# Optimization experiments

Hardware: AMD Instinct MI355X
Metric: run time of the kernel (lower is better)

Reference implementation:

```python
import jax, jax.numpy as jnp
import numpy as np

E = 8        # n_experts
TOP_K = 2    # n_activated_experts
B, T, C = 4, 2048, 2048   # batch, seq, d_model
F = 5632     # expert FFN hidden (SwiGLU)


def setup_inputs() -> dict:
    key = jax.random.key(0)
    k = jax.random.split(key, 5)
    s = 0.02  # init scale keeps activations sane
    return {
        "x":  jax.random.normal(k[0], (B, T, C), jnp.float32),
        "Wg": jax.random.normal(k[1], (C, E), jnp.float32) * s,   # gate Linear (no bias)
        "W1": jax.random.normal(k[2], (E, C, F), jnp.float32) * s, # expert gate proj
        "W3": jax.random.normal(k[3], (E, C, F), jnp.float32) * s, # expert up proj
        "W2": jax.random.normal(k[4], (E, F, C), jnp.float32) * s, # expert down proj
    }


def _moe(x, Wg, W1, W3, W2, top_k=TOP_K, norm_probs=True):
    Bb, Tt, Cc = x.shape
    xf = x.reshape(-1, Cc)                                   # [N, C]
    logits = xf @ Wg                                         # [N, E]
    probs = jax.nn.softmax(logits.astype(jnp.float32), axis=-1)
    probs, indices = jax.lax.top_k(probs, top_k)             # [N, K]
    if norm_probs:
        probs = probs / probs.sum(axis=-1, keepdims=True)
    probs = probs.astype(x.dtype)
    N, Ee = xf.shape[0], W1.shape[0]
    # per-token combine weights: w[n, e] = prob if expert e selected for token n else 0
    # (top_k indices are distinct per token, so at most one add per (n, e))
    w = jnp.zeros((N, Ee), x.dtype).at[jnp.arange(N)[:, None], indices].add(probs)
    # scan over experts: weight-0 tokens contribute nothing, matching the sparse
    # masked dispatch/scatter-add of the original exactly.
    def body(y, ws):
        w1, w3, w2, we = ws                                   # we: [N]
        h = jax.nn.silu(xf @ w1) * (xf @ w3)                  # [N, F]
        return y + we[:, None] * (h @ w2), None
    y, _ = jax.lax.scan(body, jnp.zeros_like(xf), (W1, W3, W2, w.T))
    return y.reshape(Bb, Tt, Cc)


def reference(x, Wg, W1, W3, W2):
    return _moe(x, Wg, W1, W3, W2)
```

## Files before the change

### kernel.cpp

```cpp
#include <hip/hip_runtime.h>

#define N_TOK 8192
#define C_DIM 2048
#define F_DIM 5632
#define E_NUM 8
#define BK 64

#define BM 256
#define MAXT 72
#define BN1 128
#define GRID1 (MAXT * (F_DIM/BN1))
#define BN2 256
#define KSPLIT 2
#define GRID2 (MAXT * (C_DIM/BN2) * KSPLIT)
#define NT1 (C_DIM/BK)
#define NT2H (F_DIM/BK/KSPLIT)
#define KHALF (F_DIM/KSPLIT)

typedef __attribute__((ext_vector_type(8))) short bf16x8;
typedef __attribute__((ext_vector_type(4))) float f32x4;

typedef const void __attribute__((address_space(1)))* gas1;
typedef void __attribute__((address_space(3)))* las3;

__device__ __forceinline__ unsigned short f2bf(float f){
  union { float f; unsigned u; } v; v.f = f;
  unsigned r = v.u + 0x7FFFu + ((v.u >> 16) & 1u);
  return (unsigned short)(r >> 16);
}

__device__ __forceinline__ void glds16(const unsigned short* g, unsigned short* l){
  __builtin_amdgcn_global_load_lds((gas1)g, (las3)l, 16, 0, 0);
}

#define MFMA_BF16 __builtin_amdgcn_mfma_f32_16x16x32_bf16

__global__ void k_tcvt_w(const float* __restrict__ inA, const float* __restrict__ inB,
                         unsigned short* __restrict__ out, int R, int Cc){
  __shared__ float t[64][65];
  int z = blockIdx.z;
  const float* in = (z < 8 ? inA : inB) + (size_t)(z & 7) * R * Cc;
  out += (size_t)z * R * Cc;
  int c0 = blockIdx.x * 64, r0 = blockIdx.y * 64;
  int tx = threadIdx.x, ty = threadIdx.y;
  #pragma unroll
  for (int i = 0; i < 16; ++i){
    int r = ty + i*4;
    t[r][tx] = in[(size_t)(r0 + r) * Cc + c0 + tx];
  }
  __syncthreads();
  #pragma unroll
  for (int i = 0; i < 16; ++i){
    int cr = ty + i*4;
    out[(size_t)(c0 + cr) * R + r0 + tx] = f2bf(t[tx][cr]);
  }
}

__global__ void k_router(const float* __restrict__ x, const float* __restrict__ Wg,
                         int* __restrict__ cnt, int* __restrict__ list, float* __restrict__ p_slot,
                         unsigned short* __restrict__ xb)
{
  int wid = threadIdx.x >> 6, lane = threadIdx.x & 63;
  int n = blockIdx.x * 4 + wid;
  int e = lane >> 3, sub = lane & 7;
  const float* xr = x + (size_t)n * C_DIM;
  float acc = 0.f;
  for (int i0 = sub*4; i0 < C_DIM; i0 += 32){
    float4 v = *(const float4*)&xr[i0];
    acc += v.x * Wg[(i0  )*E_NUM + e];
    acc += v.y * Wg[(i0+1)*E_NUM + e];
    acc += v.z * Wg[(i0+2)*E_NUM + e];
    acc += v.w * Wg[(i0+3)*E_NUM + e];
  }
  acc += __shfl_xor(acc, 1);
  acc += __shfl_xor(acc, 2);
  acc += __shfl_xor(acc, 4);
  float lg[E_NUM];
  #pragma unroll
  for (int j = 0; j < E_NUM; ++j) lg[j] = __shfl(acc, j*8);
  unsigned short* xbr = xb + (size_t)n * C_DIM;
  #pragma unroll
  for (int i0 = lane*4; i0 < C_DIM; i0 += 256){
    float4 v = *(const float4*)&xr[i0];
    ushort4 u; u.x = f2bf(v.x); u.y = f2bf(v.y); u.z = f2bf(v.z); u.w = f2bf(v.w);
    *(ushort4*)&xbr[i0] = u;
  }
  if (lane == 0){
    int e1 = 0; float m1 = lg[0];
    #pragma unroll
    for (int j = 1; j < E_NUM; ++j) if (lg[j] > m1){ m1 = lg[j]; e1 = j; }
    int e2 = -1; float m2 = -1e30f;
    #pragma unroll
    for (int j = 0; j < E_NUM; ++j) if (j != e1 && lg[j] > m2){ m2 = lg[j]; e2 = j; }
    float p1 = 1.f / (1.f + __expf(m2 - m1));
    float p2 = 1.f - p1;
    int pos1 = atomicAdd(&cnt[e1], 1);
    list[e1*N_TOK + pos1] = n*2;
    p_slot[n*2] = p1;
    int pos2 = atomicAdd(&cnt[e2], 1);
    list[e2*N_TOK + pos2] = n*2 + 1;
    p_slot[n*2 + 1] = p2;
  }
}

__global__ void k_prefix(const int* __restrict__ cnt, int* __restrict__ meta){
  if (threadIdx.x == 0 && blockIdx.x == 0){
    int acc = 0, t = 0;
    for (int e = 0; e < E_NUM; ++e){
      meta[e] = acc; acc += cnt[e];
      int nt = (cnt[e] + BM - 1) / BM;
      for (int i = 0; i < nt; ++i) meta[16 + t++] = (e << 16) | i;
    }
    meta[8] = t;
  }
}

#define PHASE_ENTER() do{ __builtin_amdgcn_sched_barrier(0); __builtin_amdgcn_s_barrier(); \
                          __builtin_amdgcn_s_setprio(1); } while(0)
#define PHASE_EXIT()  do{ __builtin_amdgcn_s_setprio(0); __builtin_amdgcn_sched_barrier(0); \
                          __builtin_amdgcn_s_barrier(); } while(0)

__global__ __launch_bounds__(512, 2) void k_gemm1(
    const unsigned short* __restrict__ xb,
    const unsigned short* __restrict__ wb1,
    const unsigned short* __restrict__ wb3,
    unsigned short* __restrict__ h,
    const int* __restrict__ cnt,
    const int* __restrict__ meta,
    const int* __restrict__ list)
{
  int o = blockIdx.x;
  int w = (o & 7) * (GRID1/8) + (o >> 3);
  int t = w % MAXT;
  int n0 = (w / MAXT) * BN1;
  if (t >= meta[8]) return;
  int info = meta[16 + t];
  int e  = info >> 16;
  int m0 = (info & 0xffff) * BM;
  int count = cnt[e];
  int hbase = meta[e];

  __shared__ __align__(16) unsigned short lds[2*32768];

  int tid = threadIdx.x;
  int lane = tid & 63, wid = tid >> 6;
  int wm = wid >> 1, wn = wid & 1;
  int l15 = lane & 15;
  int xc0 = (lane >> 4) ^ (lane & 7);
  int xc1 = xc0 ^ 4;

  int srow = tid >> 3;
  int swz = ((tid & 7) ^ (srow & 7)) * 8;
  const unsigned short* aP[4];
  #pragma unroll
  for (int u = 0; u < 4; ++u){
    int ts = list[e*N_TOK + m0 + u*64 + srow];
    int tok = (ts >> 1) & (N_TOK - 1);
    aP[u] = xb + (size_t)tok * C_DIM + swz;
  }
  const unsigned short* bP[4];
  #pragma unroll
  for (int u = 0; u < 4; ++u){
    const unsigned short* base = (u < 2) ? wb1 : wb3;
    bP[u] = base + ((size_t)e*F_DIM + n0 + (u & 1)*64 + srow) * C_DIM + swz;
  }
  int ldw = wid * 512;

  #define ST_A(u, kt) glds16(aP[u] + (kt)*BK, &lds[((kt)&1)*32768 + (u)*4096 + ldw])
  #define ST_B(u, kt) glds16(bP[u] + (kt)*BK, &lds[((kt)&1)*32768 + 16384 + (u)*4096 + ldw])

  ST_A(0,0); ST_A(1,0); ST_A(2,0); ST_A(3,0);
  ST_B(0,0); ST_B(1,0); ST_B(2,0); ST_B(3,0);
  ST_A(0,1); ST_A(1,1); ST_A(2,1); ST_A(3,1);
  asm volatile("s_waitcnt vmcnt(4)" ::: "memory");
  __builtin_amdgcn_sched_barrier(0);
  __builtin_amdgcn_s_barrier();

  f32x4 zero = {0.f, 0.f, 0.f, 0.f};
  f32x4 acc1[4][4], acc3[4][4];
  #pragma unroll
  for (int m = 0; m < 4; ++m)
    #pragma unroll
    for (int q = 0; q < 4; ++q){ acc1[m][q] = zero; acc3[m][q] = zero; }

  for (int kt = 0; kt < NT1; ++kt){
    const unsigned short* bufc = &lds[(kt & 1)*32768];
    bf16x8 a[4][2], b1f[2], b3f[2];
    #pragma unroll
    for (int m = 0; m < 4; ++m){
      int row = wm*64 + m*16 + l15;
      a[m][0] = *(const bf16x8*)&bufc[row*64 + xc0*8];
      a[m][1] = *(const bf16x8*)&bufc[row*64 + xc1*8];
    }
    {
      int brow = wn*64 + l15;
      b1f[0] = *(const bf16x8*)&bufc[16384 + brow*64 + xc0*8];
      b1f[1] = *(const bf16x8*)&bufc[16384 + brow*64 + xc1*8];
      b3f[0] = *(const bf16x8*)&bufc[24576 + brow*64 + xc0*8];
      b3f[1] = *(const bf16x8*)&bufc[24576 + brow*64 + xc1*8];
    }
    ST_B(0, kt+1); ST_B(1, kt+1); ST_B(2, kt+1); ST_B(3, kt+1);
    PHASE_ENTER();
    #pragma unroll
    for (int m = 0; m < 4; ++m){
      acc1[m][0] = MFMA_BF16(a[m][0], b1f[0], acc1[m][0], 0, 0, 0);
      acc1[m][0] = MFMA_BF16(a[m][1], b1f[1], acc1[m][0], 0, 0, 0);
      acc3[m][0] = MFMA_BF16(a[m][0], b3f[0], acc3[m][0], 0, 0, 0);
      acc3[m][0] = MFMA_BF16(a[m][1], b3f[1], acc3[m][0], 0, 0, 0);
    }
    PHASE_EXIT();
    #pragma unroll
    for (int q = 1; q < 4; ++q){
      int brow = wn*64 + q*16 + l15;
      b1f[0] = *(const bf16x8*)&bufc[16384 + brow*64 + xc0*8];
      b1f[1] = *(const bf16x8*)&bufc[16384 + brow*64 + xc1*8];
      b3f[0] = *(const bf16x8*)&bufc[24576 + brow*64 + xc0*8];
      b3f[1] = *(const bf16x8*)&bufc[24576 + brow*64 + xc1*8];
      if (q == 1){ ST_A(0, kt+2); ST_A(1, kt+2); }
      if (q == 2){ ST_A(2, kt+2); ST_A(3, kt+2); }
      PHASE_ENTER();
      #pragma unroll
      for (int m = 0; m < 4; ++m){
        acc1[m][q] = MFMA_BF16(a[m][0], b1f[0], acc1[m][q], 0, 0, 0);
        acc1[m][q] = MFMA_BF16(a[m][1], b1f[1], acc1[m][q], 0, 0, 0);
        acc3[m][q] = MFMA_BF16(a[m][0], b3f[0], acc3[m][q], 0, 0, 0);
        acc3[m][q] = MFMA_BF16(a[m][1], b3f[1], acc3[m][q], 0, 0, 0);
      }
      __builtin_amdgcn_s_setprio(0);
      if (q == 3) asm volatile("s_waitcnt vmcnt(4)" ::: "memory");
      __builtin_amdgcn_sched_barrier(0);
      __builtin_amdgcn_s_barrier();
    }
  }
  asm volatile("s_waitcnt vmcnt(0)" ::: "memory");

  #pragma unroll
  for (int m = 0; m < 4; ++m){
    #pragma unroll
    for (int r = 0; r < 4; ++r){
      int rloc = m0 + wm*64 + m*16 + ((lane >> 4) * 4) + r;
      if (rloc < count){
        unsigned short* hrow = h + (size_t)(hbase + rloc) * F_DIM + n0 + wn*64 + l15;
        #pragma unroll
        for (int q = 0; q < 4; ++q){
          float v1 = acc1[m][q][r];
          float v3 = acc3[m][q][r];
          float hv = (v1 / (1.f + __expf(-v1))) * v3;
          hrow[q*16] = f2bf(hv);
        }
      }
    }
  }
  #undef ST_A
  #undef ST_B
}

__global__ __launch_bounds__(512, 2) void k_gemm2(
    const unsigned short* __restrict__ h,
    const unsigned short* __restrict__ wb2,
    float* __restrict__ y,
    const int* __restrict__ cnt,
    const int* __restrict__ meta,
    const int* __restrict__ list,
    const float* __restrict__ p_slot)
{
  int o = blockIdx.x;
  int w = (o & 7) * (GRID2/8) + (o >> 3);
  int ks = w / (GRID2/KSPLIT);
  int r2 = w % (GRID2/KSPLIT);
  int t = r2 % MAXT;
  int n0 = (r2 / MAXT) * BN2;
  if (t >= meta[8]) return;
  int info = meta[16 + t];
  int e  = info >> 16;
  int m0 = (info & 0xffff) * BM;
  int count = cnt[e];
  int hbase = meta[e];

  __shared__ __align__(16) unsigned short lds[2*32768];

  int tid = threadIdx.x;
  int lane = tid & 63, wid = tid >> 6;
  int wm = wid >> 1, wn = wid & 1;
  int l15 = lane & 15;
  int xc0 = (lane >> 4) ^ (lane & 7);
  int xc1 = xc0 ^ 4;

  int srow = tid >> 3;
  int swz = ((tid & 7) ^ (srow & 7)) * 8;
  size_t kb0 = (size_t)ks * KHALF;
  const unsigned short* aP[4];
  #pragma unroll
  for (int u = 0; u < 4; ++u)
    aP[u] = h + (size_t)(hbase + m0 + u*64 + srow) * F_DIM + kb0 + swz;
  const unsigned short* bP[4];
  #pragma unroll
  for (int u = 0; u < 4; ++u)
    bP[u] = wb2 + ((size_t)e*C_DIM + n0 + u*64 + srow) * F_DIM + kb0 + swz;
  int ldw = wid * 512;

  #define ST_A2(u, kt) glds16(aP[u] + (kt)*BK, &lds[((kt)&1)*32768 + (u)*4096 + ldw])
  #define ST_B2(u, kt) glds16(bP[u] + (kt)*BK, &lds[((kt)&1)*32768 + 16384 + (u)*4096 + ldw])

  ST_A2(0,0); ST_A2(1,0); ST_A2(2,0); ST_A2(3,0);
  ST_B2(0,0); ST_B2(1,0); ST_B2(2,0); ST_B2(3,0);
  asm volatile("s_waitcnt vmcnt(4)" ::: "memory");
  ST_A2(0,1); ST_A2(1,1); ST_A2(2,1); ST_A2(3,1);
  ST_B2(0,1); ST_B2(2,1);
  asm volatile("s_waitcnt vmcnt(6)" ::: "memory");
  __builtin_amdgcn_sched_barrier(0);
  __builtin_amdgcn_s_barrier();

  f32x4 zero = {0.f, 0.f, 0.f, 0.f};
  f32x4 acc[4][8];
  #pragma unroll
  for (int m = 0; m < 4; ++m)
    #pragma unroll
    for (int nf = 0; nf < 8; ++nf) acc[m][nf] = zero;

  for (int kt = 0; kt < NT2H; ++kt){
    const unsigned short* bufc = &lds[(kt & 1)*32768];
    bf16x8 a[4][2], bf[2][2];
    #pragma unroll
    for (int m = 0; m < 4; ++m){
      int row = wm*64 + m*16 + l15;
      a[m][0] = *(const bf16x8*)&bufc[row*64 + xc0*8];
      a[m][1] = *(const bf16x8*)&bufc[row*64 + xc1*8];
    }
    #pragma unroll
    for (int j = 0; j < 2; ++j){
      int brow = wn*128 + j*16 + l15;
      bf[j][0] = *(const bf16x8*)&bufc[16384 + brow*64 + xc0*8];
      bf[j][1] = *(const bf16x8*)&bufc[16384 + brow*64 + xc1*8];
    }
    ST_B2(1, kt+1); ST_B2(3, kt+1);
    PHASE_ENTER();
    #pragma unroll
    for (int m = 0; m < 4; ++m)
      #pragma unroll
      for (int j = 0; j < 2; ++j){
        acc[m][j] = MFMA_BF16(a[m][0], bf[j][0], acc[m][j], 0, 0, 0);
        acc[m][j] = MFMA_BF16(a[m][1], bf[j][1], acc[m][j], 0, 0, 0);
      }
    PHASE_EXIT();
    #pragma unroll
    for (int q = 1; q < 4; ++q){
      #pragma unroll
      for (int j = 0; j < 2; ++j){
        int brow = wn*128 + (q*2 + j)*16 + l15;
        bf[j][0] = *(const bf16x8*)&bufc[16384 + brow*64 + xc0*8];
        bf[j][1] = *(const bf16x8*)&bufc[16384 + brow*64 + xc1*8];
      }
      if (q == 1){ ST_A2(0, kt+2); ST_A2(1, kt+2); }
      if (q == 2){ ST_A2(2, kt+2); ST_A2(3, kt+2); }
      if (q == 3){ ST_B2(0, kt+2); ST_B2(2, kt+2); }
      PHASE_ENTER();
      #pragma unroll
      for (int m = 0; m < 4; ++m)
        #pragma unroll
        for (int j = 0; j < 2; ++j){
          acc[m][q*2+j] = MFMA_BF16(a[m][0], bf[j][0], acc[m][q*2+j], 0, 0, 0);
          acc[m][q*2+j] = MFMA_BF16(a[m][1], bf[j][1], acc[m][q*2+j], 0, 0, 0);
        }
      __builtin_amdgcn_s_setprio(0);
      if (q == 3) asm volatile("s_waitcnt vmcnt(6)" ::: "memory");
      __builtin_amdgcn_sched_barrier(0);
      __builtin_amdgcn_s_barrier();
    }
  }
  asm volatile("s_waitcnt vmcnt(0)" ::: "memory");

  #pragma unroll
  for (int m = 0; m < 4; ++m){
    #pragma unroll
    for (int r = 0; r < 4; ++r){
      int rloc = m0 + wm*64 + m*16 + ((lane >> 4) * 4) + r;
      if (rloc < count){
        int ts = list[e*N_TOK + rloc];
        float p = p_slot[ts];
        int tok = ts >> 1;
        float* yr = y + (size_t)tok * C_DIM + n0 + wn*128 + l15;
        #pragma unroll
        for (int nf = 0; nf < 8; ++nf)
          atomicAdd(&yr[nf*16], p * acc[m][nf][r]);
      }
    }
  }
  #undef ST_A2
  #undef ST_B2
}

extern "C" void kernel_launch(void* const* d_in, const int* in_sizes, int n_in,
                              void* d_out, int out_size, void* d_ws, size_t ws_size,
                              hipStream_t stream)
{
  const float* x  = (const float*)d_in[0];
  const float* Wg = (const float*)d_in[1];
  const float* W1 = (const float*)d_in[2];
  const float* W3 = (const float*)d_in[3];
  const float* W2 = (const float*)d_in[4];
  float* y = (float*)d_out;
  (void)in_sizes; (void)n_in; (void)out_size; (void)ws_size;

  char* ws = (char*)d_ws;
  size_t o = 0;
  auto alloc = [&](size_t bytes)->char* {
    char* p = ws + o;
    o = (o + bytes + 255) & ~(size_t)255;
    return p;
  };
  int*    cnt    = (int*)  alloc(E_NUM * 4);
  int*    meta   = (int*)  alloc(160 * 4);
  float*  p_slot = (float*)alloc((size_t)2*N_TOK * 4);
  int*    list   = (int*)  alloc((size_t)E_NUM*N_TOK * 4);
  unsigned short* xb  = (unsigned short*)alloc((size_t)N_TOK*C_DIM * 2);
  unsigned short* wb1 = (unsigned short*)alloc((size_t)E_NUM*C_DIM*F_DIM * 2);
  unsigned short* wb3 = (unsigned short*)alloc((size_t)E_NUM*C_DIM*F_DIM * 2);
  unsigned short* wb2 = (unsigned short*)alloc((size_t)E_NUM*C_DIM*F_DIM * 2);
  unsigned short* h   = (unsigned short*)alloc((size_t)(2*N_TOK + 1024)*F_DIM * 2);
  (void)wb3;

  hipMemsetAsync(cnt, 0, E_NUM * 4, stream);
  hipMemsetAsync(y, 0, (size_t)N_TOK * C_DIM * 4, stream);
  k_router<<<N_TOK/4, 256, 0, stream>>>(x, Wg, cnt, list, p_slot, xb);
  k_prefix<<<1, 64, 0, stream>>>(cnt, meta);
  k_tcvt_w<<<dim3(F_DIM/64, C_DIM/64, 2*E_NUM), dim3(64,4), 0, stream>>>(W1, W3, wb1, C_DIM, F_DIM);
  k_tcvt_w<<<dim3(C_DIM/64, F_DIM/64, E_NUM), dim3(64,4), 0, stream>>>(W2, W2, wb2, F_DIM, C_DIM);
  k_gemm1<<<GRID1, 512, 0, stream>>>(xb, wb1, wb3, h, cnt, meta, list);
  k_gemm2<<<GRID2, 512, 0, stream>>>(h, wb2, y, cnt, meta, list, p_slot);
}
```

Baseline: 1.834 ms.

## Fuse preprocessing kernels, overlap W2 conversion with GEMM1, prefetch A fragments

The router, the y zeroing and the W1/W3 transpose-convert now run as one launch, replacing a memset and three kernels. The W2 transpose-convert is appended as extra blocks of the GEMM1 grid so it can overlap with the expert GEMM work. Both GEMM main loops now load the next tile's A fragments from LDS during the last sub-phase and carry them in registers across iterations, which adds register pressure and moves one B prefetch in GEMM2. Packing the conversion blocks after the GEMM blocks depends on the block scheduler running them alongside the GEMM blocks.

```diff
diff --git a/kernel.cpp b/kernel.cpp
--- a/kernel.cpp
+++ b/kernel.cpp
@@ -17,6 +17,13 @@
 #define NT2H (F_DIM/BK/KSPLIT)
 #define KHALF (F_DIM/KSPLIT)
 
+#define PRE_R 2048
+#define PRE_Y 4096
+#define PRE_T 45056
+#define GRID_PRE (PRE_R + PRE_Y + PRE_T)
+#define G1_TCVT 22528
+#define GRID1F (GRID1 + G1_TCVT)
+
 typedef __attribute__((ext_vector_type(8))) short bf16x8;
 typedef __attribute__((ext_vector_type(4))) float f32x4;
 
@@ -35,71 +42,87 @@
 
 #define MFMA_BF16 __builtin_amdgcn_mfma_f32_16x16x32_bf16
 
-__global__ void k_tcvt_w(const float* __restrict__ inA, const float* __restrict__ inB,
-                         unsigned short* __restrict__ out, int R, int Cc){
+__global__ __launch_bounds__(256) void k_pre(
+    const float* __restrict__ x, const float* __restrict__ Wg,
+    const float* __restrict__ W1, const float* __restrict__ W3,
+    int* __restrict__ cnt, int* __restrict__ list, float* __restrict__ p_slot,
+    unsigned short* __restrict__ xb, unsigned short* __restrict__ wb13,
+    float* __restrict__ y)
+{
   __shared__ float t[64][65];
-  int z = blockIdx.z;
-  const float* in = (z < 8 ? inA : inB) + (size_t)(z & 7) * R * Cc;
-  out += (size_t)z * R * Cc;
-  int c0 = blockIdx.x * 64, r0 = blockIdx.y * 64;
-  int tx = threadIdx.x, ty = threadIdx.y;
+  int bid = blockIdx.x;
+  int tid = threadIdx.x;
+
+  if (bid < PRE_R){
+    int wid = tid >> 6, lane = tid & 63;
+    int n = bid * 4 + wid;
+    int e = lane >> 3, sub = lane & 7;
+    const float* xr = x + (size_t)n * C_DIM;
+    float acc = 0.f;
+    for (int i0 = sub*4; i0 < C_DIM; i0 += 32){
+      float4 v = *(const float4*)&xr[i0];
+      acc += v.x * Wg[(i0  )*E_NUM + e];
+      acc += v.y * Wg[(i0+1)*E_NUM + e];
+      acc += v.z * Wg[(i0+2)*E_NUM + e];
+      acc += v.w * Wg[(i0+3)*E_NUM + e];
+    }
+    acc += __shfl_xor(acc, 1);
+    acc += __shfl_xor(acc, 2);
+    acc += __shfl_xor(acc, 4);
+    float lg[E_NUM];
+    #pragma unroll
+    for (int j = 0; j < E_NUM; ++j) lg[j] = __shfl(acc, j*8);
+    unsigned short* xbr = xb + (size_t)n * C_DIM;
+    #pragma unroll
+    for (int i0 = lane*4; i0 < C_DIM; i0 += 256){
+      float4 v = *(const float4*)&xr[i0];
+      ushort4 u; u.x = f2bf(v.x); u.y = f2bf(v.y); u.z = f2bf(v.z); u.w = f2bf(v.w);
+      *(ushort4*)&xbr[i0] = u;
+    }
+    if (lane == 0){
+      int e1 = 0; float m1 = lg[0];
+      #pragma unroll
+      for (int j = 1; j < E_NUM; ++j) if (lg[j] > m1){ m1 = lg[j]; e1 = j; }
+      int e2 = -1; float m2 = -1e30f;
+      #pragma unroll
+      for (int j = 0; j < E_NUM; ++j) if (j != e1 && lg[j] > m2){ m2 = lg[j]; e2 = j; }
+      float p1 = 1.f / (1.f + __expf(m2 - m1));
+      float p2 = 1.f - p1;
+      int pos1 = atomicAdd(&cnt[e1], 1);
+      list[e1*N_TOK + pos1] = n*2;
+      p_slot[n*2] = p1;
+      int pos2 = atomicAdd(&cnt[e2], 1);
+      list[e2*N_TOK + pos2] = n*2 + 1;
+      p_slot[n*2 + 1] = p2;
+    }
+    return;
+  }
+  if (bid < PRE_R + PRE_Y){
+    float4* y4 = (float4*)y;
+    size_t base = (size_t)(bid - PRE_R) * 1024 + tid;
+    float4 z4 = {0.f, 0.f, 0.f, 0.f};
+    #pragma unroll
+    for (int j = 0; j < 4; ++j) y4[base + j*256] = z4;
+    return;
+  }
+  int rel = bid - (PRE_R + PRE_Y);
+  int z = rel / 2816;
+  int r2 = rel - z*2816;
+  int fx = r2 % 88, cy = r2 / 88;
+  const float* in = ((z < 8) ? W1 : W3) + (size_t)(z & 7) * C_DIM * F_DIM;
+  unsigned short* out = wb13 + (size_t)z * C_DIM * F_DIM;
+  int c0 = fx*64, r0 = cy*64;
+  int tx = tid & 63, ty = tid >> 6;
   #pragma unroll
   for (int i = 0; i < 16; ++i){
     int r = ty + i*4;
-    t[r][tx] = in[(size_t)(r0 + r) * Cc + c0 + tx];
+    t[r][tx] = in[(size_t)(r0 + r) * F_DIM + c0 + tx];
   }
   __syncthreads();
   #pragma unroll
   for (int i = 0; i < 16; ++i){
     int cr = ty + i*4;
-    out[(size_t)(c0 + cr) * R + r0 + tx] = f2bf(t[tx][cr]);
-  }
-}
-
-__global__ void k_router(const float* __restrict__ x, const float* __restrict__ Wg,
-                         int* __restrict__ cnt, int* __restrict__ list, float* __restrict__ p_slot,
-                         unsigned short* __restrict__ xb)
-{
-  int wid = threadIdx.x >> 6, lane = threadIdx.x & 63;
-  int n = blockIdx.x * 4 + wid;
-  int e = lane >> 3, sub = lane & 7;
-  const float* xr = x + (size_t)n * C_DIM;
-  float acc = 0.f;
-  for (int i0 = sub*4; i0 < C_DIM; i0 += 32){
-    float4 v = *(const float4*)&xr[i0];
-    acc += v.x * Wg[(i0  )*E_NUM + e];
-    acc += v.y * Wg[(i0+1)*E_NUM + e];
-    acc += v.z * Wg[(i0+2)*E_NUM + e];
-    acc += v.w * Wg[(i0+3)*E_NUM + e];
-  }
-  acc += __shfl_xor(acc, 1);
-  acc += __shfl_xor(acc, 2);
-  acc += __shfl_xor(acc, 4);
-  float lg[E_NUM];
-  #pragma unroll
-  for (int j = 0; j < E_NUM; ++j) lg[j] = __shfl(acc, j*8);
-  unsigned short* xbr = xb + (size_t)n * C_DIM;
-  #pragma unroll
-  for (int i0 = lane*4; i0 < C_DIM; i0 += 256){
-    float4 v = *(const float4*)&xr[i0];
-    ushort4 u; u.x = f2bf(v.x); u.y = f2bf(v.y); u.z = f2bf(v.z); u.w = f2bf(v.w);
-    *(ushort4*)&xbr[i0] = u;
-  }
-  if (lane == 0){
-    int e1 = 0; float m1 = lg[0];
-    #pragma unroll
-    for (int j = 1; j < E_NUM; ++j) if (lg[j] > m1){ m1 = lg[j]; e1 = j; }
-    int e2 = -1; float m2 = -1e30f;
-    #pragma unroll
-    for (int j = 0; j < E_NUM; ++j) if (j != e1 && lg[j] > m2){ m2 = lg[j]; e2 = j; }
-    float p1 = 1.f / (1.f + __expf(m2 - m1));
-    float p2 = 1.f - p1;
-    int pos1 = atomicAdd(&cnt[e1], 1);
-    list[e1*N_TOK + pos1] = n*2;
-    p_slot[n*2] = p1;
-    int pos2 = atomicAdd(&cnt[e2], 1);
-    list[e2*N_TOK + pos2] = n*2 + 1;
-    p_slot[n*2 + 1] = p2;
+    out[(size_t)(c0 + cr) * C_DIM + r0 + tx] = f2bf(t[tx][cr]);
   }
 }
 
@@ -127,9 +150,38 @@
     unsigned short* __restrict__ h,
     const int* __restrict__ cnt,
     const int* __restrict__ meta,
-    const int* __restrict__ list)
+    const int* __restrict__ list,
+    const float* __restrict__ W2,
+    unsigned short* __restrict__ wb2)
 {
+  __shared__ __align__(16) unsigned short lds[2*32768];
   int o = blockIdx.x;
+  int tid = threadIdx.x;
+
+  if (o >= GRID1){
+    float (*t)[65] = (float(*)[65])lds;
+    int rel = o - GRID1;
+    int z = rel / 2816;
+    int r2 = rel - z*2816;
+    int cx = r2 % 32, fy = r2 / 32;
+    const float* in = W2 + (size_t)z * F_DIM * C_DIM;
+    unsigned short* out = wb2 + (size_t)z * C_DIM * F_DIM;
+    int c0 = cx*64, r0 = fy*64;
+    int tx = tid & 63, ty = tid >> 6;
+    #pragma unroll
+    for (int i = 0; i < 8; ++i){
+      int r = ty + i*8;
+      t[r][tx] = in[(size_t)(r0 + r) * C_DIM + c0 + tx];
+    }
+    __syncthreads();
+    #pragma unroll
+    for (int i = 0; i < 8; ++i){
+      int cr = ty + i*8;
+      out[(size_t)(c0 + cr) * F_DIM + r0 + tx] = f2bf(t[tx][cr]);
+    }
+    return;
+  }
+
   int w = (o & 7) * (GRID1/8) + (o >> 3);
   int t = w % MAXT;
   int n0 = (w / MAXT) * BN1;
@@ -140,9 +192,6 @@
   int count = cnt[e];
   int hbase = meta[e];
 
-  __shared__ __align__(16) unsigned short lds[2*32768];
-
-  int tid = threadIdx.x;
   int lane = tid & 63, wid = tid >> 6;
   int wm = wid >> 1, wn = wid & 1;
   int l15 = lane & 15;
@@ -183,15 +232,18 @@
     #pragma unroll
     for (int q = 0; q < 4; ++q){ acc1[m][q] = zero; acc3[m][q] = zero; }
 
+  bf16x8 a[4][2];
+  #pragma unroll
+  for (int m = 0; m < 4; ++m){
+    int row = wm*64 + m*16 + l15;
+    a[m][0] = *(const bf16x8*)&lds[row*64 + xc0*8];
+    a[m][1] = *(const bf16x8*)&lds[row*64 + xc1*8];
+  }
+
   for (int kt = 0; kt < NT1; ++kt){
     const unsigned short* bufc = &lds[(kt & 1)*32768];
-    bf16x8 a[4][2], b1f[2], b3f[2];
-    #pragma unroll
-    for (int m = 0; m < 4; ++m){
-      int row = wm*64 + m*16 + l15;
-      a[m][0] = *(const bf16x8*)&bufc[row*64 + xc0*8];
-      a[m][1] = *(const bf16x8*)&bufc[row*64 + xc1*8];
-    }
+    const unsigned short* bufn = &lds[((kt+1) & 1)*32768];
+    bf16x8 b1f[2], b3f[2];
     {
       int brow = wn*64 + l15;
       b1f[0] = *(const bf16x8*)&bufc[16384 + brow*64 + xc0*8];
@@ -210,14 +262,14 @@
     }
     PHASE_EXIT();
     #pragma unroll
-    for (int q = 1; q < 4; ++q){
+    for (int q = 1; q < 3; ++q){
       int brow = wn*64 + q*16 + l15;
       b1f[0] = *(const bf16x8*)&bufc[16384 + brow*64 + xc0*8];
       b1f[1] = *(const bf16x8*)&bufc[16384 + brow*64 + xc1*8];
       b3f[0] = *(const bf16x8*)&bufc[24576 + brow*64 + xc0*8];
       b3f[1] = *(const bf16x8*)&bufc[24576 + brow*64 + xc1*8];
       if (q == 1){ ST_A(0, kt+2); ST_A(1, kt+2); }
-      if (q == 2){ ST_A(2, kt+2); ST_A(3, kt+2); }
+      else       { ST_A(2, kt+2); ST_A(3, kt+2); }
       PHASE_ENTER();
       #pragma unroll
       for (int m = 0; m < 4; ++m){
@@ -226,11 +278,36 @@
         acc3[m][q] = MFMA_BF16(a[m][0], b3f[0], acc3[m][q], 0, 0, 0);
         acc3[m][q] = MFMA_BF16(a[m][1], b3f[1], acc3[m][q], 0, 0, 0);
       }
-      __builtin_amdgcn_s_setprio(0);
-      if (q == 3) asm volatile("s_waitcnt vmcnt(4)" ::: "memory");
-      __builtin_amdgcn_sched_barrier(0);
-      __builtin_amdgcn_s_barrier();
-    }
+      PHASE_EXIT();
+    }
+    {
+      int brow = wn*64 + 3*16 + l15;
+      b1f[0] = *(const bf16x8*)&bufc[16384 + brow*64 + xc0*8];
+      b1f[1] = *(const bf16x8*)&bufc[16384 + brow*64 + xc1*8];
+      b3f[0] = *(const bf16x8*)&bufc[24576 + brow*64 + xc0*8];
+      b3f[1] = *(const bf16x8*)&bufc[24576 + brow*64 + xc1*8];
+    }
+    asm volatile("s_waitcnt vmcnt(4)" ::: "memory");
+    __builtin_amdgcn_sched_barrier(0);
+    __builtin_amdgcn_s_barrier();
+    __builtin_amdgcn_s_setprio(1);
+    bf16x8 an[4][2];
+    #pragma unroll
+    for (int m = 0; m < 4; ++m){
+      int row = wm*64 + m*16 + l15;
+      an[m][0] = *(const bf16x8*)&bufn[row*64 + xc0*8];
+      an[m][1] = *(const bf16x8*)&bufn[row*64 + xc1*8];
+    }
+    #pragma unroll
+    for (int m = 0; m < 4; ++m){
+      acc1[m][3] = MFMA_BF16(a[m][0], b1f[0], acc1[m][3], 0, 0, 0);
+      acc1[m][3] = MFMA_BF16(a[m][1], b1f[1], acc1[m][3], 0, 0, 0);
+      acc3[m][3] = MFMA_BF16(a[m][0], b3f[0], acc3[m][3], 0, 0, 0);
+      acc3[m][3] = MFMA_BF16(a[m][1], b3f[1], acc3[m][3], 0, 0, 0);
+    }
+    PHASE_EXIT();
+    #pragma unroll
+    for (int m = 0; m < 4; ++m){ a[m][0] = an[m][0]; a[m][1] = an[m][1]; }
   }
   asm volatile("s_waitcnt vmcnt(0)" ::: "memory");
 
@@ -318,15 +395,18 @@
     #pragma unroll
     for (int nf = 0; nf < 8; ++nf) acc[m][nf] = zero;
 
+  bf16x8 a[4][2];
+  #pragma unroll
+  for (int m = 0; m < 4; ++m){
+    int row = wm*64 + m*16 + l15;
+    a[m][0] = *(const bf16x8*)&lds[row*64 + xc0*8];
+    a[m][1] = *(const bf16x8*)&lds[row*64 + xc1*8];
+  }
+
   for (int kt = 0; kt < NT2H; ++kt){
     const unsigned short* bufc = &lds[(kt & 1)*32768];
-    bf16x8 a[4][2], bf[2][2];
-    #pragma unroll
-    for (int m = 0; m < 4; ++m){
-      int row = wm*64 + m*16 + l15;
-      a[m][0] = *(const bf16x8*)&bufc[row*64 + xc0*8];
-      a[m][1] = *(const bf16x8*)&bufc[row*64 + xc1*8];
-    }
+    const unsigned short* bufn = &lds[((kt+1) & 1)*32768];
+    bf16x8 bf[2][2];
     #pragma unroll
     for (int j = 0; j < 2; ++j){
       int brow = wn*128 + j*16 + l15;
@@ -344,7 +424,7 @@
       }
     PHASE_EXIT();
     #pragma unroll
-    for (int q = 1; q < 4; ++q){
+    for (int q = 1; q < 3; ++q){
       #pragma unroll
       for (int j = 0; j < 2; ++j){
         int brow = wn*128 + (q*2 + j)*16 + l15;
@@ -352,8 +432,7 @@
         bf[j][1] = *(const bf16x8*)&bufc[16384 + brow*64 + xc1*8];
       }
       if (q == 1){ ST_A2(0, kt+2); ST_A2(1, kt+2); }
-      if (q == 2){ ST_A2(2, kt+2); ST_A2(3, kt+2); }
-      if (q == 3){ ST_B2(0, kt+2); ST_B2(2, kt+2); }
+      else       { ST_A2(2, kt+2); ST_A2(3, kt+2); }
       PHASE_ENTER();
       #pragma unroll
       for (int m = 0; m < 4; ++m)
@@ -362,11 +441,36 @@
           acc[m][q*2+j] = MFMA_BF16(a[m][0], bf[j][0], acc[m][q*2+j], 0, 0, 0);
           acc[m][q*2+j] = MFMA_BF16(a[m][1], bf[j][1], acc[m][q*2+j], 0, 0, 0);
         }
-      __builtin_amdgcn_s_setprio(0);
-      if (q == 3) asm volatile("s_waitcnt vmcnt(6)" ::: "memory");
-      __builtin_amdgcn_sched_barrier(0);
-      __builtin_amdgcn_s_barrier();
-    }
+      PHASE_EXIT();
+    }
+    #pragma unroll
+    for (int j = 0; j < 2; ++j){
+      int brow = wn*128 + (6 + j)*16 + l15;
+      bf[j][0] = *(const bf16x8*)&bufc[16384 + brow*64 + xc0*8];
+      bf[j][1] = *(const bf16x8*)&bufc[16384 + brow*64 + xc1*8];
+    }
+    ST_B2(0, kt+2); ST_B2(2, kt+2);
+    asm volatile("s_waitcnt vmcnt(6)" ::: "memory");
+    __builtin_amdgcn_sched_barrier(0);
+    __builtin_amdgcn_s_barrier();
+    __builtin_amdgcn_s_setprio(1);
+    bf16x8 an[4][2];
+    #pragma unroll
+    for (int m = 0; m < 4; ++m){
+      int row = wm*64 + m*16 + l15;
+      an[m][0] = *(const bf16x8*)&bufn[row*64 + xc0*8];
+      an[m][1] = *(const bf16x8*)&bufn[row*64 + xc1*8];
+    }
+    #pragma unroll
+    for (int m = 0; m < 4; ++m)
+      #pragma unroll
+      for (int j = 0; j < 2; ++j){
+        acc[m][6+j] = MFMA_BF16(a[m][0], bf[j][0], acc[m][6+j], 0, 0, 0);
+        acc[m][6+j] = MFMA_BF16(a[m][1], bf[j][1], acc[m][6+j], 0, 0, 0);
+      }
+    PHASE_EXIT();
+    #pragma unroll
+    for (int m = 0; m < 4; ++m){ a[m][0] = an[m][0]; a[m][1] = an[m][1]; }
   }
   asm volatile("s_waitcnt vmcnt(0)" ::: "memory");
 
@@ -421,11 +525,8 @@
   (void)wb3;
 
   hipMemsetAsync(cnt, 0, E_NUM * 4, stream);
-  hipMemsetAsync(y, 0, (size_t)N_TOK * C_DIM * 4, stream);
-  k_router<<<N_TOK/4, 256, 0, stream>>>(x, Wg, cnt, list, p_slot, xb);
+  k_pre<<<GRID_PRE, 256, 0, stream>>>(x, Wg, W1, W3, cnt, list, p_slot, xb, wb1, y);
   k_prefix<<<1, 64, 0, stream>>>(cnt, meta);
-  k_tcvt_w<<<dim3(F_DIM/64, C_DIM/64, 2*E_NUM), dim3(64,4), 0, stream>>>(W1, W3, wb1, C_DIM, F_DIM);
-  k_tcvt_w<<<dim3(C_DIM/64, F_DIM/64, E_NUM), dim3(64,4), 0, stream>>>(W2, W2, wb2, F_DIM, C_DIM);
-  k_gemm1<<<GRID1, 512, 0, stream>>>(xb, wb1, wb3, h, cnt, meta, list);
+  k_gemm1<<<GRID1F, 512, 0, stream>>>(xb, wb1, wb3, h, cnt, meta, list, W2, wb2);
   k_gemm2<<<GRID2, 512, 0, stream>>>(h, wb2, y, cnt, meta, list, p_slot);
 }
```

After: 1.842 ms. Within noise of the previous version (+0.5%).

## Fuse router, output zeroing and W1/W3 transpose; software-pipeline LDS fragment reads in GEMMs

Applied to the files above, without the earlier changes.

Merges the router, the y memset and the W1/W3 bf16 transpose into one launch, so these independent prep jobs can run concurrently and launch overhead drops. In both GEMM kernels, the LDS fragment reads are now double-buffered in registers: the next B slice (and the next tile's A) is read while MFMAs run on the current one. This hides LDS latency behind matrix math, at the cost of more live registers, which may pressure occupancy under the 512x2 launch bounds.

```diff
diff --git a/kernel.cpp b/kernel.cpp
--- a/kernel.cpp
+++ b/kernel.cpp
@@ -17,6 +17,11 @@
 #define NT2H (F_DIM/BK/KSPLIT)
 #define KHALF (F_DIM/KSPLIT)
 
+#define PRE_R 2048
+#define PRE_Y 4096
+#define PRE_T 45056
+#define GRID_PRE (PRE_R + PRE_Y + PRE_T)
+
 typedef __attribute__((ext_vector_type(8))) short bf16x8;
 typedef __attribute__((ext_vector_type(4))) float f32x4;
 
@@ -35,71 +40,106 @@
 
 #define MFMA_BF16 __builtin_amdgcn_mfma_f32_16x16x32_bf16
 
-__global__ void k_tcvt_w(const float* __restrict__ inA, const float* __restrict__ inB,
-                         unsigned short* __restrict__ out, int R, int Cc){
+__global__ __launch_bounds__(256) void k_pre(
+    const float* __restrict__ x, const float* __restrict__ Wg,
+    const float* __restrict__ W1, const float* __restrict__ W3,
+    int* __restrict__ cnt, int* __restrict__ list, float* __restrict__ p_slot,
+    unsigned short* __restrict__ xb, unsigned short* __restrict__ wb13,
+    float* __restrict__ y)
+{
   __shared__ float t[64][65];
-  int z = blockIdx.z;
-  const float* in = (z < 8 ? inA : inB) + (size_t)(z & 7) * R * Cc;
-  out += (size_t)z * R * Cc;
+  int bid = blockIdx.x;
+  int tid = threadIdx.x;
+
+  if (bid < PRE_R){
+    int wid = tid >> 6, lane = tid & 63;
+    int n = bid * 4 + wid;
+    int e = lane >> 3, sub = lane & 7;
+    const float* xr = x + (size_t)n * C_DIM;
+    float acc = 0.f;
+    for (int i0 = sub*4; i0 < C_DIM; i0 += 32){
+      float4 v = *(const float4*)&xr[i0];
+      acc += v.x * Wg[(i0  )*E_NUM + e];
+      acc += v.y * Wg[(i0+1)*E_NUM + e];
+      acc += v.z * Wg[(i0+2)*E_NUM + e];
+      acc += v.w * Wg[(i0+3)*E_NUM + e];
+    }
+    acc += __shfl_xor(acc, 1);
+    acc += __shfl_xor(acc, 2);
+    acc += __shfl_xor(acc, 4);
+    float lg[E_NUM];
+    #pragma unroll
+    for (int j = 0; j < E_NUM; ++j) lg[j] = __shfl(acc, j*8);
+    unsigned short* xbr = xb + (size_t)n * C_DIM;
+    #pragma unroll
+    for (int i0 = lane*4; i0 < C_DIM; i0 += 256){
+      float4 v = *(const float4*)&xr[i0];
+      ushort4 u; u.x = f2bf(v.x); u.y = f2bf(v.y); u.z = f2bf(v.z); u.w = f2bf(v.w);
+      *(ushort4*)&xbr[i0] = u;
+    }
+    if (lane == 0){
+      int e1 = 0; float m1 = lg[0];
+      #pragma unroll
+      for (int j = 1; j < E_NUM; ++j) if (lg[j] > m1){ m1 = lg[j]; e1 = j; }
+      int e2 = -1; float m2 = -1e30f;
+      #pragma unroll
+      for (int j = 0; j < E_NUM; ++j) if (j != e1 && lg[j] > m2){ m2 = lg[j]; e2 = j; }
+      float p1 = 1.f / (1.f + __expf(m2 - m1));
+      float p2 = 1.f - p1;
+      int pos1 = atomicAdd(&cnt[e1], 1);
+      list[e1*N_TOK + pos1] = n*2;
+      p_slot[n*2] = p1;
+      int pos2 = atomicAdd(&cnt[e2], 1);
+      list[e2*N_TOK + pos2] = n*2 + 1;
+      p_slot[n*2 + 1] = p2;
+    }
+    return;
+  }
+  if (bid < PRE_R + PRE_Y){
+    float4* y4 = (float4*)y;
+    size_t base = (size_t)(bid - PRE_R) * 1024 + tid;
+    float4 z4 = {0.f, 0.f, 0.f, 0.f};
+    #pragma unroll
+    for (int j = 0; j < 4; ++j) y4[base + j*256] = z4;
+    return;
+  }
+  int rel = bid - (PRE_R + PRE_Y);
+  int z = rel / 2816;
+  int r2 = rel - z*2816;
+  int fx = r2 % 88, cy = r2 / 88;
+  const float* in = ((z < 8) ? W1 : W3) + (size_t)(z & 7) * C_DIM * F_DIM;
+  unsigned short* out = wb13 + (size_t)z * C_DIM * F_DIM;
+  int c0 = fx*64, r0 = cy*64;
+  int tx = tid & 63, ty = tid >> 6;
+  #pragma unroll
+  for (int i = 0; i < 16; ++i){
+    int r = ty + i*4;
+    t[r][tx] = in[(size_t)(r0 + r) * F_DIM + c0 + tx];
+  }
+  __syncthreads();
+  #pragma unroll
+  for (int i = 0; i < 16; ++i){
+    int cr = ty + i*4;
+    out[(size_t)(c0 + cr) * C_DIM + r0 + tx] = f2bf(t[tx][cr]);
+  }
+}
+
+__global__ void k_tw2(const float* __restrict__ W2, unsigned short* __restrict__ wb2){
+  __shared__ float t[64][65];
+  const float* in = W2 + (size_t)blockIdx.z * F_DIM * C_DIM;
+  unsigned short* out = wb2 + (size_t)blockIdx.z * C_DIM * F_DIM;
   int c0 = blockIdx.x * 64, r0 = blockIdx.y * 64;
   int tx = threadIdx.x, ty = threadIdx.y;
   #pragma unroll
   for (int i = 0; i < 16; ++i){
     int r = ty + i*4;
-    t[r][tx] = in[(size_t)(r0 + r) * Cc + c0 + tx];
+    t[r][tx] = in[(size_t)(r0 + r) * C_DIM + c0 + tx];
   }
   __syncthreads();
   #pragma unroll
   for (int i = 0; i < 16; ++i){
     int cr = ty + i*4;
-    out[(size_t)(c0 + cr) * R + r0 + tx] = f2bf(t[tx][cr]);
-  }
-}
-
-__global__ void k_router(const float* __restrict__ x, const float* __restrict__ Wg,
-                         int* __restrict__ cnt, int* __restrict__ list, float* __restrict__ p_slot,
-                         unsigned short* __restrict__ xb)
-{
-  int wid = threadIdx.x >> 6, lane = threadIdx.x & 63;
-  int n = blockIdx.x * 4 + wid;
-  int e = lane >> 3, sub = lane & 7;
-  const float* xr = x + (size_t)n * C_DIM;
-  float acc = 0.f;
-  for (int i0 = sub*4; i0 < C_DIM; i0 += 32){
-    float4 v = *(const float4*)&xr[i0];
-    acc += v.x * Wg[(i0  )*E_NUM + e];
-    acc += v.y * Wg[(i0+1)*E_NUM + e];
-    acc += v.z * Wg[(i0+2)*E_NUM + e];
-    acc += v.w * Wg[(i0+3)*E_NUM + e];
-  }
-  acc += __shfl_xor(acc, 1);
-  acc += __shfl_xor(acc, 2);
-  acc += __shfl_xor(acc, 4);
-  float lg[E_NUM];
-  #pragma unroll
-  for (int j = 0; j < E_NUM; ++j) lg[j] = __shfl(acc, j*8);
-  unsigned short* xbr = xb + (size_t)n * C_DIM;
-  #pragma unroll
-  for (int i0 = lane*4; i0 < C_DIM; i0 += 256){
-    float4 v = *(const float4*)&xr[i0];
-    ushort4 u; u.x = f2bf(v.x); u.y = f2bf(v.y); u.z = f2bf(v.z); u.w = f2bf(v.w);
-    *(ushort4*)&xbr[i0] = u;
-  }
-  if (lane == 0){
-    int e1 = 0; float m1 = lg[0];
-    #pragma unroll
-    for (int j = 1; j < E_NUM; ++j) if (lg[j] > m1){ m1 = lg[j]; e1 = j; }
-    int e2 = -1; float m2 = -1e30f;
-    #pragma unroll
-    for (int j = 0; j < E_NUM; ++j) if (j != e1 && lg[j] > m2){ m2 = lg[j]; e2 = j; }
-    float p1 = 1.f / (1.f + __expf(m2 - m1));
-    float p2 = 1.f - p1;
-    int pos1 = atomicAdd(&cnt[e1], 1);
-    list[e1*N_TOK + pos1] = n*2;
-    p_slot[n*2] = p1;
-    int pos2 = atomicAdd(&cnt[e2], 1);
-    list[e2*N_TOK + pos2] = n*2 + 1;
-    p_slot[n*2 + 1] = p2;
+    out[(size_t)(c0 + cr) * F_DIM + r0 + tx] = f2bf(t[tx][cr]);
   }
 }
 
@@ -129,7 +169,10 @@
     const int* __restrict__ meta,
     const int* __restrict__ list)
 {
+  __shared__ __align__(16) unsigned short lds[2*32768];
   int o = blockIdx.x;
+  int tid = threadIdx.x;
+
   int w = (o & 7) * (GRID1/8) + (o >> 3);
   int t = w % MAXT;
   int n0 = (w / MAXT) * BN1;
@@ -140,9 +183,6 @@
   int count = cnt[e];
   int hbase = meta[e];
 
-  __shared__ __align__(16) unsigned short lds[2*32768];
-
-  int tid = threadIdx.x;
   int lane = tid & 63, wid = tid >> 6;
   int wm = wid >> 1, wn = wid & 1;
   int l15 = lane & 15;
@@ -168,6 +208,20 @@
 
   #define ST_A(u, kt) glds16(aP[u] + (kt)*BK, &lds[((kt)&1)*32768 + (u)*4096 + ldw])
   #define ST_B(u, kt) glds16(bP[u] + (kt)*BK, &lds[((kt)&1)*32768 + 16384 + (u)*4096 + ldw])
+  #define READ_A(d, buf) do{ _Pragma("unroll") for (int m_ = 0; m_ < 4; ++m_){ \
+      int row_ = wm*64 + m_*16 + l15; \
+      d[m_][0] = *(const bf16x8*)&(buf)[row_*64 + xc0*8]; \
+      d[m_][1] = *(const bf16x8*)&(buf)[row_*64 + xc1*8]; } }while(0)
+  #define READ_B(d1, d3, buf, q) do{ int brow_ = wn*64 + (q)*16 + l15; \
+      d1[0] = *(const bf16x8*)&(buf)[16384 + brow_*64 + xc0*8]; \
+      d1[1] = *(const bf16x8*)&(buf)[16384 + brow_*64 + xc1*8]; \
+      d3[0] = *(const bf16x8*)&(buf)[24576 + brow_*64 + xc0*8]; \
+      d3[1] = *(const bf16x8*)&(buf)[24576 + brow_*64 + xc1*8]; }while(0)
+  #define MFMA16(q, b1, b3) do{ _Pragma("unroll") for (int m_ = 0; m_ < 4; ++m_){ \
+      acc1[m_][q] = MFMA_BF16(a[m_][0], b1[0], acc1[m_][q], 0, 0, 0); \
+      acc1[m_][q] = MFMA_BF16(a[m_][1], b1[1], acc1[m_][q], 0, 0, 0); \
+      acc3[m_][q] = MFMA_BF16(a[m_][0], b3[0], acc3[m_][q], 0, 0, 0); \
+      acc3[m_][q] = MFMA_BF16(a[m_][1], b3[1], acc3[m_][q], 0, 0, 0); } }while(0)
 
   ST_A(0,0); ST_A(1,0); ST_A(2,0); ST_A(3,0);
   ST_B(0,0); ST_B(1,0); ST_B(2,0); ST_B(3,0);
@@ -183,54 +237,38 @@
     #pragma unroll
     for (int q = 0; q < 4; ++q){ acc1[m][q] = zero; acc3[m][q] = zero; }
 
+  bf16x8 a[4][2];
+  READ_A(a, lds);
+  bf16x8 bX1[2], bX3[2], bY1[2], bY3[2];
+  READ_B(bX1, bX3, lds, 0);
+
   for (int kt = 0; kt < NT1; ++kt){
     const unsigned short* bufc = &lds[(kt & 1)*32768];
-    bf16x8 a[4][2], b1f[2], b3f[2];
-    #pragma unroll
-    for (int m = 0; m < 4; ++m){
-      int row = wm*64 + m*16 + l15;
-      a[m][0] = *(const bf16x8*)&bufc[row*64 + xc0*8];
-      a[m][1] = *(const bf16x8*)&bufc[row*64 + xc1*8];
-    }
-    {
-      int brow = wn*64 + l15;
-      b1f[0] = *(const bf16x8*)&bufc[16384 + brow*64 + xc0*8];
-      b1f[1] = *(const bf16x8*)&bufc[16384 + brow*64 + xc1*8];
-      b3f[0] = *(const bf16x8*)&bufc[24576 + brow*64 + xc0*8];
-      b3f[1] = *(const bf16x8*)&bufc[24576 + brow*64 + xc1*8];
-    }
+    const unsigned short* bufn = &lds[((kt+1) & 1)*32768];
     ST_B(0, kt+1); ST_B(1, kt+1); ST_B(2, kt+1); ST_B(3, kt+1);
     PHASE_ENTER();
-    #pragma unroll
-    for (int m = 0; m < 4; ++m){
-      acc1[m][0] = MFMA_BF16(a[m][0], b1f[0], acc1[m][0], 0, 0, 0);
-      acc1[m][0] = MFMA_BF16(a[m][1], b1f[1], acc1[m][0], 0, 0, 0);
-      acc3[m][0] = MFMA_BF16(a[m][0], b3f[0], acc3[m][0], 0, 0, 0);
-      acc3[m][0] = MFMA_BF16(a[m][1], b3f[1], acc3[m][0], 0, 0, 0);
-    }
-    PHASE_EXIT();
-    #pragma unroll
-    for (int q = 1; q < 4; ++q){
-      int brow = wn*64 + q*16 + l15;
-      b1f[0] = *(const bf16x8*)&bufc[16384 + brow*64 + xc0*8];
-      b1f[1] = *(const bf16x8*)&bufc[16384 + brow*64 + xc1*8];
-      b3f[0] = *(const bf16x8*)&bufc[24576 + brow*64 + xc0*8];
-      b3f[1] = *(const bf16x8*)&bufc[24576 + brow*64 + xc1*8];
-      if (q == 1){ ST_A(0, kt+2); ST_A(1, kt+2); }
-      if (q == 2){ ST_A(2, kt+2); ST_A(3, kt+2); }
-      PHASE_ENTER();
-      #pragma unroll
-      for (int m = 0; m < 4; ++m){
-        acc1[m][q] = MFMA_BF16(a[m][0], b1f[0], acc1[m][q], 0, 0, 0);
-        acc1[m][q] = MFMA_BF16(a[m][1], b1f[1], acc1[m][q], 0, 0, 0);
-        acc3[m][q] = MFMA_BF16(a[m][0], b3f[0], acc3[m][q], 0, 0, 0);
-        acc3[m][q] = MFMA_BF16(a[m][1], b3f[1], acc3[m][q], 0, 0, 0);
-      }
-      __builtin_amdgcn_s_setprio(0);
-      if (q == 3) asm volatile("s_waitcnt vmcnt(4)" ::: "memory");
-      __builtin_amdgcn_sched_barrier(0);
-      __builtin_amdgcn_s_barrier();
-    }
+    READ_B(bY1, bY3, bufc, 1);
+    MFMA16(0, bX1, bX3);
+    PHASE_EXIT();
+    ST_A(0, kt+2); ST_A(1, kt+2);
+    PHASE_ENTER();
+    READ_B(bX1, bX3, bufc, 2);
+    MFMA16(1, bY1, bY3);
+    PHASE_EXIT();
+    ST_A(2, kt+2); ST_A(3, kt+2);
+    PHASE_ENTER();
+    READ_B(bY1, bY3, bufc, 3);
+    MFMA16(2, bX1, bX3);
+    PHASE_EXIT();
+    asm volatile("s_waitcnt vmcnt(4)" ::: "memory");
+    PHASE_ENTER();
+    bf16x8 an[4][2];
+    READ_A(an, bufn);
+    READ_B(bX1, bX3, bufn, 0);
+    MFMA16(3, bY1, bY3);
+    PHASE_EXIT();
+    #pragma unroll
+    for (int m = 0; m < 4; ++m){ a[m][0] = an[m][0]; a[m][1] = an[m][1]; }
   }
   asm volatile("s_waitcnt vmcnt(0)" ::: "memory");
 
@@ -253,6 +291,9 @@
   }
   #undef ST_A
   #undef ST_B
+  #undef READ_A
+  #undef READ_B
+  #undef MFMA16
 }
 
 __global__ __launch_bounds__(512, 2) void k_gemm2(
@@ -301,6 +342,18 @@
 
   #define ST_A2(u, kt) glds16(aP[u] + (kt)*BK, &lds[((kt)&1)*32768 + (u)*4096 + ldw])
   #define ST_B2(u, kt) glds16(bP[u] + (kt)*BK, &lds[((kt)&1)*32768 + 16384 + (u)*4096 + ldw])
+  #define READ_A2(d, buf) do{ _Pragma("unroll") for (int m_ = 0; m_ < 4; ++m_){ \
+      int row_ = wm*64 + m_*16 + l15; \
+      d[m_][0] = *(const bf16x8*)&(buf)[row_*64 + xc0*8]; \
+      d[m_][1] = *(const bf16x8*)&(buf)[row_*64 + xc1*8]; } }while(0)
+  #define READ_B2(d, buf, q) do{ _Pragma("unroll") for (int j_ = 0; j_ < 2; ++j_){ \
+      int brow_ = wn*128 + ((q)*2 + j_)*16 + l15; \
+      d[j_][0] = *(const bf16x8*)&(buf)[16384 + brow_*64 + xc0*8]; \
+      d[j_][1] = *(const bf16x8*)&(buf)[16384 + brow_*64 + xc1*8]; } }while(0)
+  #define MFMA2(qb, d) do{ _Pragma("unroll") for (int m_ = 0; m_ < 4; ++m_) \
+      _Pragma("unroll") for (int j_ = 0; j_ < 2; ++j_){ \
+        acc[m_][(qb)*2+j_] = MFMA_BF16(a[m_][0], d[j_][0], acc[m_][(qb)*2+j_], 0, 0, 0); \
+        acc[m_][(qb)*2+j_] = MFMA_BF16(a[m_][1], d[j_][1], acc[m_][(qb)*2+j_], 0, 0, 0); } }while(0)
 
   ST_A2(0,0); ST_A2(1,0); ST_A2(2,0); ST_A2(3,0);
   ST_B2(0,0); ST_B2(1,0); ST_B2(2,0); ST_B2(3,0);
@@ -318,55 +371,39 @@
     #pragma unroll
     for (int nf = 0; nf < 8; ++nf) acc[m][nf] = zero;
 
+  bf16x8 a[4][2];
+  READ_A2(a, lds);
+  bf16x8 bfX[2][2], bfY[2][2];
+  READ_B2(bfX, lds, 0);
+
   for (int kt = 0; kt < NT2H; ++kt){
     const unsigned short* bufc = &lds[(kt & 1)*32768];
-    bf16x8 a[4][2], bf[2][2];
-    #pragma unroll
-    for (int m = 0; m < 4; ++m){
-      int row = wm*64 + m*16 + l15;
-      a[m][0] = *(const bf16x8*)&bufc[row*64 + xc0*8];
-      a[m][1] = *(const bf16x8*)&bufc[row*64 + xc1*8];
-    }
-    #pragma unroll
-    for (int j = 0; j < 2; ++j){
-      int brow = wn*128 + j*16 + l15;
-      bf[j][0] = *(const bf16x8*)&bufc[16384 + brow*64 + xc0*8];
-      bf[j][1] = *(const bf16x8*)&bufc[16384 + brow*64 + xc1*8];
-    }
+    const unsigned short* bufn = &lds[((kt+1) & 1)*32768];
     ST_B2(1, kt+1); ST_B2(3, kt+1);
     PHASE_ENTER();
-    #pragma unroll
-    for (int m = 0; m < 4; ++m)
-      #pragma unroll
-      for (int j = 0; j < 2; ++j){
-        acc[m][j] = MFMA_BF16(a[m][0], bf[j][0], acc[m][j], 0, 0, 0);
-        acc[m][j] = MFMA_BF16(a[m][1], bf[j][1], acc[m][j], 0, 0, 0);
-      }
-    PHASE_EXIT();
-    #pragma unroll
-    for (int q = 1; q < 4; ++q){
-      #pragma unroll
-      for (int j = 0; j < 2; ++j){
-        int brow = wn*128 + (q*2 + j)*16 + l15;
-        bf[j][0] = *(const bf16x8*)&bufc[16384 + brow*64 + xc0*8];
-        bf[j][1] = *(const bf16x8*)&bufc[16384 + brow*64 + xc1*8];
-      }
-      if (q == 1){ ST_A2(0, kt+2); ST_A2(1, kt+2); }
-      if (q == 2){ ST_A2(2, kt+2); ST_A2(3, kt+2); }
-      if (q == 3){ ST_B2(0, kt+2); ST_B2(2, kt+2); }
-      PHASE_ENTER();
-      #pragma unroll
-      for (int m = 0; m < 4; ++m)
-        #pragma unroll
-        for (int j = 0; j < 2; ++j){
-          acc[m][q*2+j] = MFMA_BF16(a[m][0], bf[j][0], acc[m][q*2+j], 0, 0, 0);
-          acc[m][q*2+j] = MFMA_BF16(a[m][1], bf[j][1], acc[m][q*2+j], 0, 0, 0);
-        }
-      __builtin_amdgcn_s_setprio(0);
-      if (q == 3) asm volatile("s_waitcnt vmcnt(6)" ::: "memory");
-      __builtin_amdgcn_sched_barrier(0);
-      __builtin_amdgcn_s_barrier();
-    }
+    READ_B2(bfY, bufc, 1);
+    MFMA2(0, bfX);
+    PHASE_EXIT();
+    ST_A2(0, kt+2); ST_A2(1, kt+2);
+    PHASE_ENTER();
+    READ_B2(bfX, bufc, 2);
+    MFMA2(1, bfY);
+    PHASE_EXIT();
+    ST_A2(2, kt+2); ST_A2(3, kt+2);
+    PHASE_ENTER();
+    READ_B2(bfY, bufc, 3);
+    MFMA2(2, bfX);
+    PHASE_EXIT();
+    ST_B2(0, kt+2); ST_B2(2, kt+2);
+    asm volatile("s_waitcnt vmcnt(6)" ::: "memory");
+    PHASE_ENTER();
+    bf16x8 an[4][2];
+    READ_A2(an, bufn);
+    READ_B2(bfX, bufn, 0);
+    MFMA2(3, bfY);
+    PHASE_EXIT();
+    #pragma unroll
+    for (int m = 0; m < 4; ++m){ a[m][0] = an[m][0]; a[m][1] = an[m][1]; }
   }
   asm volatile("s_waitcnt vmcnt(0)" ::: "memory");
 
@@ -388,6 +425,9 @@
   }
   #undef ST_A2
   #undef ST_B2
+  #undef READ_A2
+  #undef READ_B2
+  #undef MFMA2
 }
 
 extern "C" void kernel_launch(void* const* d_in, const int* in_sizes, int n_in,
@@ -421,11 +461,9 @@
   (void)wb3;
 
   hipMemsetAsync(cnt, 0, E_NUM * 4, stream);
-  hipMemsetAsync(y, 0, (size_t)N_TOK * C_DIM * 4, stream);
-  k_router<<<N_TOK/4, 256, 0, stream>>>(x, Wg, cnt, list, p_slot, xb);
+  k_pre<<<GRID_PRE, 256, 0, stream>>>(x, Wg, W1, W3, cnt, list, p_slot, xb, wb1, y);
   k_prefix<<<1, 64, 0, stream>>>(cnt, meta);
-  k_tcvt_w<<<dim3(F_DIM/64, C_DIM/64, 2*E_NUM), dim3(64,4), 0, stream>>>(W1, W3, wb1, C_DIM, F_DIM);
-  k_tcvt_w<<<dim3(C_DIM/64, F_DIM/64, E_NUM), dim3(64,4), 0, stream>>>(W2, W2, wb2, F_DIM, C_DIM);
+  k_tw2<<<dim3(C_DIM/64, F_DIM/64, E_NUM), dim3(64,4), 0, stream>>>(W2, wb2);
   k_gemm1<<<GRID1, 512, 0, stream>>>(xb, wb1, wb3, h, cnt, meta, list);
   k_gemm2<<<GRID2, 512, 0, stream>>>(h, wb2, y, cnt, meta, list, p_slot);
 }
```

New measurement: 1.830 ms. Within noise of the previous version (-0.2%).
